# Kernel optimization log

Measured on AMD Instinct MI355X. Metric: run time of the kernel, lower is better.

The kernel has to match this reference:

```python
import jax, jax.numpy as jnp
import numpy as np

L = 8          # number of QTT cores = log2(init_reso)
RESO = 256     # init_reso
MAX_RANK = 256
N_SAMPLES = 4096


def _qtt_ranks(L, max_rank):
    return [min(8 ** k, 8 ** (L - k), max_rank) for k in range(L + 1)]


def setup_inputs() -> dict:
    key = jax.random.key(0)
    ranks = _qtt_ranks(L, MAX_RANK)
    keys = jax.random.split(key, L + 1)
    inp = {}
    for l in range(L):
        shape = (ranks[l], 8, ranks[l + 1])
        scale = (shape[0] * shape[1]) ** -0.5  # keep chain products O(1)
        inp[f"core{l}"] = jax.random.normal(keys[l], shape, dtype=jnp.float32) * scale
    inp["coords_xyz"] = jax.random.randint(keys[L], (N_SAMPLES, 3), 0, RESO)
    return inp


def _coords_to_qtt(coords_xyz, num_cores):
    # coords_xyz: (N, 3) int. Per core l (most-significant bit first):
    # c_l = 4*bit_x + 2*bit_y + bit_z in [0, 8)  -> shape (L, N)
    x, y, z = coords_xyz[:, 0], coords_xyz[:, 1], coords_xyz[:, 2]
    shifts = jnp.arange(num_cores - 1, -1, -1)[:, None]  # (L, 1)
    bx = (x[None, :] >> shifts) & 1
    by = (y[None, :] >> shifts) & 1
    bz = (z[None, :] >> shifts) & 1
    return 4 * bx + 2 * by + bz


def _sample_tt(cores, coords):
    # cores[l]: (r_l, 8, r_{l+1}); coords: (L, N)
    # v starts as first core slice: (N, r_1)  (r_0 == 1)
    v = cores[0][0, coords[0], :]
    for l in range(1, len(cores)):
        # gathered slice: (r_l, N, r_{l+1}) -> (N, r_l, r_{l+1})
        g = jnp.transpose(cores[l][:, coords[l], :], (1, 0, 2))
        v = jnp.einsum('nr,nrs->ns', v, g)
    return v[:, 0]  # r_L == 1 -> (N,)


def reference(core0, core1, core2, core3, core4, core5, core6, core7, coords_xyz):
    cores = [core0, core1, core2, core3, core4, core5, core6, core7]
    coords = _coords_to_qtt(coords_xyz, len(cores))
    return _sample_tt(cores, coords)
```

## Files before the change

kernel.cpp:

```cpp
#include <hip/hip_runtime.h>


typedef unsigned int u32;

__device__ __forceinline__ void fma4(float4& c, float a, const float4& b) {
    c.x = fmaf(a, b.x, c.x); c.y = fmaf(a, b.y, c.y);
    c.z = fmaf(a, b.z, c.z); c.w = fmaf(a, b.w, c.w);
}
__device__ __forceinline__ int digit_of(int x, int y, int z, int sh) {
    return 4*((x>>sh)&1) + 2*((y>>sh)&1) + ((z>>sh)&1);
}

__global__ __launch_bounds__(256, 4) void prep_kernel(
    const float* __restrict__ C4, float* __restrict__ C4t)
{
    const int t = threadIdx.x;
    const int cb = blockIdx.x;
    const int d4 = cb >> 3, s5o = cb & 7;
#pragma unroll 8
    for (int j = 0; j < 32; ++j) {
        const int s5 = s5o*32 + j;
        C4t[(size_t)d4*65536 + (size_t)s5*256 + t] =
            C4[(size_t)t*2048 + d4*256 + s5];
    }
}

__device__ __forceinline__ void comp8(
    const float (*As)[260], int kk,
    const float4& b0, const float4& b1, const float4& b2, const float4& b3,
    float4* acc)
{
#pragma unroll
    for (int r = 0; r < 8; ++r) {
        const float4 a = *(const float4*)&As[r][kk];
        fma4(acc[r], a.x, b0); fma4(acc[r], a.y, b1);
        fma4(acc[r], a.z, b2); fma4(acc[r], a.w, b3);
    }
}

template<int ROWSTRIDE>
__device__ __forceinline__ void kgemm8(
    const float* __restrict__ Bg,
    const float (*As)[260], int kbase, int ln, float4* acc)
{
    const float* gp = Bg + (size_t)kbase * ROWSTRIDE + (size_t)ln * 4;
    float4 bA0 = *(const float4*)(gp + (size_t)0*ROWSTRIDE);
    float4 bA1 = *(const float4*)(gp + (size_t)1*ROWSTRIDE);
    float4 bA2 = *(const float4*)(gp + (size_t)2*ROWSTRIDE);
    float4 bA3 = *(const float4*)(gp + (size_t)3*ROWSTRIDE);
    float4 bB0 = *(const float4*)(gp + (size_t)4*ROWSTRIDE);
    float4 bB1 = *(const float4*)(gp + (size_t)5*ROWSTRIDE);
    float4 bB2 = *(const float4*)(gp + (size_t)6*ROWSTRIDE);
    float4 bB3 = *(const float4*)(gp + (size_t)7*ROWSTRIDE);

#pragma unroll 1
    for (int s = 0; s < 8; ++s) {
        const int k0 = s * 8;
        comp8(As, kbase + k0, bA0, bA1, bA2, bA3, acc);
        if (s < 7) {
            bA0 = *(const float4*)(gp + (size_t)(k0+ 8)*ROWSTRIDE);
            bA1 = *(const float4*)(gp + (size_t)(k0+ 9)*ROWSTRIDE);
            bA2 = *(const float4*)(gp + (size_t)(k0+10)*ROWSTRIDE);
            bA3 = *(const float4*)(gp + (size_t)(k0+11)*ROWSTRIDE);
        }
        comp8(As, kbase + k0 + 4, bB0, bB1, bB2, bB3, acc);
        if (s < 7) {
            bB0 = *(const float4*)(gp + (size_t)(k0+12)*ROWSTRIDE);
            bB1 = *(const float4*)(gp + (size_t)(k0+13)*ROWSTRIDE);
            bB2 = *(const float4*)(gp + (size_t)(k0+14)*ROWSTRIDE);
            bB3 = *(const float4*)(gp + (size_t)(k0+15)*ROWSTRIDE);
        }
    }
}

__global__ __launch_bounds__(256, 2) void tables_kernel(
    const float* __restrict__ C0, const float* __restrict__ C1,
    const float* __restrict__ C2, const float* __restrict__ C3,
    const float* __restrict__ C4t, const float* __restrict__ C5,
    const float* __restrict__ C6, const float* __restrict__ C7,
    float* __restrict__ P3, float* __restrict__ U)
{
    __shared__ __align__(16) union {
        struct { float small[8][64]; float As[8][260]; } g;
        float red[4][4][256];
    } u;
    const int t = threadIdx.x;
    const int ln = t & 63, wv = t >> 6;
    const int bx = blockIdx.x;

    float4 acc[8];
#pragma unroll
    for (int r = 0; r < 8; ++r) acc[r] = make_float4(0,0,0,0);

    int rowBase, rowStep;
    float* outP;

    if (bx < 512) {
        const int d3 = bx & 7, d2 = (bx >> 3) & 7, d0 = bx >> 6;

#pragma unroll
        for (int j = 0; j < 2; ++j) {
            const int idx = t + 256*j, d1 = idx >> 6, c = idx & 63;
            float a = 0.f;
#pragma unroll
            for (int r8 = 0; r8 < 8; ++r8)
                a = fmaf(C0[d0*8 + r8], C1[r8*512 + d1*64 + c], a);
            u.g.small[d1][c] = a;
        }
        __syncthreads();

        {
            float4 a0 = make_float4(0,0,0,0), a1 = make_float4(0,0,0,0);
            const float* c2base = C2 + d2*256 + ln*4;
#pragma unroll 8
            for (int j = 0; j < 64; ++j) {
                const float4 c2 = *(const float4*)(c2base + (size_t)j*2048);
                fma4(a0, u.g.small[wv*2 + 0][j], c2);
                fma4(a1, u.g.small[wv*2 + 1][j], c2);
            }
            *(float4*)&u.g.As[wv*2 + 0][ln*4] = a0;
            *(float4*)&u.g.As[wv*2 + 1][ln*4] = a1;
        }
        __syncthreads();

        kgemm8<2048>(C3 + d3*256, u.g.As, wv*64, ln, acc);

        rowBase = d0*512 + d2*8 + d3; rowStep = 64;
        outP = P3;
    } else {
        const int ub = bx - 512;
        const int qt = ub & 63, d4 = ub >> 6;
        const int d5 = qt >> 3, d6 = qt & 7;

#pragma unroll
        for (int j = 0; j < 2; ++j) {
            const int idx = t + 256*j, r = idx >> 6, s6 = idx & 63;
            float a = 0.f;
#pragma unroll
            for (int jj = 0; jj < 8; ++jj)
                a = fmaf(C6[s6*64 + d6*8 + jj], C7[jj*8 + r], a);
            u.g.small[r][s6] = a;
        }
        __syncthreads();

        {
            float accT[8];
#pragma unroll
            for (int r = 0; r < 8; ++r) accT[r] = 0.f;
#pragma unroll
            for (int j4 = 0; j4 < 16; ++j4) {
                const float4 c5 = *(const float4*)(C5 + (size_t)t*512
                                                   + d5*64 + j4*4);
#pragma unroll
                for (int r = 0; r < 8; ++r) {
                    const float4 s6v = *(const float4*)&u.g.small[r][j4*4];
                    accT[r] = fmaf(c5.x, s6v.x, accT[r]);
                    accT[r] = fmaf(c5.y, s6v.y, accT[r]);
                    accT[r] = fmaf(c5.z, s6v.z, accT[r]);
                    accT[r] = fmaf(c5.w, s6v.w, accT[r]);
                }
            }
#pragma unroll
            for (int r = 0; r < 8; ++r) u.g.As[r][t] = accT[r];
        }
        __syncthreads();

        kgemm8<256>(C4t + (size_t)d4*65536, u.g.As, wv*64, ln, acc);

        rowBase = d4*512 + qt*8; rowStep = 1;
        outP = U;
    }

    __syncthreads();

#pragma unroll
    for (int ph = 0; ph < 2; ++ph) {
#pragma unroll
        for (int i = 0; i < 4; ++i)
            *(float4*)&u.red[wv][i][ln*4] = acc[ph*4 + i];
        __syncthreads();
        {
            float4 v        = *(const float4*)&u.red[0][wv][ln*4];
            const float4 p1 = *(const float4*)&u.red[1][wv][ln*4];
            const float4 p2 = *(const float4*)&u.red[2][wv][ln*4];
            const float4 p3 = *(const float4*)&u.red[3][wv][ln*4];
            v.x += p1.x + p2.x + p3.x; v.y += p1.y + p2.y + p3.y;
            v.z += p1.z + p2.z + p3.z; v.w += p1.w + p2.w + p3.w;
            const int r = ph*4 + wv;
            *(float4*)(outP + (size_t)(rowBase + rowStep*r)*256 + ln*4) = v;
        }
        __syncthreads();
    }
}

__global__ __launch_bounds__(256) void final_kernel(
    const float* __restrict__ P3, const float* __restrict__ U,
    const int* __restrict__ coords, int n, float* __restrict__ out)
{
    const int ln = threadIdx.x & 63, wv = threadIdx.x >> 6;
    const int s0 = blockIdx.x * 16 + wv * 4;

    float p[4] = {0.f, 0.f, 0.f, 0.f};
    int valid[4];
#pragma unroll
    for (int i = 0; i < 4; ++i) {
        const int s = s0 + i;
        valid[i] = (s < n);
        if (valid[i]) {
            const int x = coords[3*s], y = coords[3*s+1], z = coords[3*s+2];
            const int a  = digit_of(x,y,z,7)*512 + digit_of(x,y,z,6)*64
                         + digit_of(x,y,z,5)*8  + digit_of(x,y,z,4);
            const int d4 = digit_of(x,y,z,3);
            const int q  = digit_of(x,y,z,2)*64 + digit_of(x,y,z,1)*8
                         + digit_of(x,y,z,0);
            const float4 p4 = *(const float4*)(P3 + (size_t)a*256 + ln*4);
            const float4 u4 = *(const float4*)(U + (size_t)(d4*512 + q)*256 + ln*4);
            p[i] = fmaf(p4.x, u4.x, fmaf(p4.y, u4.y,
                   fmaf(p4.z, u4.z, p4.w * u4.w)));
        }
    }
#pragma unroll
    for (int m = 1; m <= 32; m <<= 1) {
        p[0] += __shfl_xor(p[0], m);
        p[1] += __shfl_xor(p[1], m);
        p[2] += __shfl_xor(p[2], m);
        p[3] += __shfl_xor(p[3], m);
    }
    if (ln == 0) {
#pragma unroll
        for (int i = 0; i < 4; ++i)
            if (valid[i]) out[s0 + i] = p[i];
    }
}

extern "C" void kernel_launch(void* const* d_in, const int* in_sizes, int n_in,
                              void* d_out, int out_size, void* d_ws, size_t ws_size,
                              hipStream_t stream) {
    const float* C0 = (const float*)d_in[0];
    const float* C1 = (const float*)d_in[1];
    const float* C2 = (const float*)d_in[2];
    const float* C3 = (const float*)d_in[3];
    const float* C4 = (const float*)d_in[4];
    const float* C5 = (const float*)d_in[5];
    const float* C6 = (const float*)d_in[6];
    const float* C7 = (const float*)d_in[7];
    const int* coords = (const int*)d_in[8];
    float* out = (float*)d_out;

    const int n = in_sizes[8] / 3;

    float* P3  = (float*)d_ws;
    float* U   = P3 + 4096*256;
    float* C4t = U  + 4096*256;

    prep_kernel<<<64, 256, 0, stream>>>(C4, C4t);
    tables_kernel<<<1024, 256, 0, stream>>>(
        C0, C1, C2, C3, C4t, C5, C6, C7, P3, U);
    final_kernel<<<(n + 15) / 16, 256, 0, stream>>>(P3, U, coords, n, out);
}
```

Baseline: 107.0 us.

## Split tables kernel output columns in half to double block count

```diff
diff --git a/kernel.cpp b/kernel.cpp
--- a/kernel.cpp
+++ b/kernel.cpp
@@ -6,6 +6,9 @@
 __device__ __forceinline__ void fma4(float4& c, float a, const float4& b) {
     c.x = fmaf(a, b.x, c.x); c.y = fmaf(a, b.y, c.y);
     c.z = fmaf(a, b.z, c.z); c.w = fmaf(a, b.w, c.w);
+}
+__device__ __forceinline__ void fma2(float2& c, float a, const float2& b) {
+    c.x = fmaf(a, b.x, c.x); c.y = fmaf(a, b.y, c.y);
 }
 __device__ __forceinline__ int digit_of(int x, int y, int z, int sh) {
     return 4*((x>>sh)&1) + 2*((y>>sh)&1) + ((z>>sh)&1);
@@ -25,50 +28,50 @@
     }
 }
 
-__device__ __forceinline__ void comp8(
+__device__ __forceinline__ void comp8h(
     const float (*As)[260], int kk,
-    const float4& b0, const float4& b1, const float4& b2, const float4& b3,
-    float4* acc)
+    const float2& b0, const float2& b1, const float2& b2, const float2& b3,
+    float2* acc)
 {
 #pragma unroll
     for (int r = 0; r < 8; ++r) {
         const float4 a = *(const float4*)&As[r][kk];
-        fma4(acc[r], a.x, b0); fma4(acc[r], a.y, b1);
-        fma4(acc[r], a.z, b2); fma4(acc[r], a.w, b3);
+        fma2(acc[r], a.x, b0); fma2(acc[r], a.y, b1);
+        fma2(acc[r], a.z, b2); fma2(acc[r], a.w, b3);
     }
 }
 
 template<int ROWSTRIDE>
-__device__ __forceinline__ void kgemm8(
-    const float* __restrict__ Bg,
-    const float (*As)[260], int kbase, int ln, float4* acc)
-{
-    const float* gp = Bg + (size_t)kbase * ROWSTRIDE + (size_t)ln * 4;
-    float4 bA0 = *(const float4*)(gp + (size_t)0*ROWSTRIDE);
-    float4 bA1 = *(const float4*)(gp + (size_t)1*ROWSTRIDE);
-    float4 bA2 = *(const float4*)(gp + (size_t)2*ROWSTRIDE);
-    float4 bA3 = *(const float4*)(gp + (size_t)3*ROWSTRIDE);
-    float4 bB0 = *(const float4*)(gp + (size_t)4*ROWSTRIDE);
-    float4 bB1 = *(const float4*)(gp + (size_t)5*ROWSTRIDE);
-    float4 bB2 = *(const float4*)(gp + (size_t)6*ROWSTRIDE);
-    float4 bB3 = *(const float4*)(gp + (size_t)7*ROWSTRIDE);
+__device__ __forceinline__ void kgemm8h(
+    const float* __restrict__ Bg, int colOff,
+    const float (*As)[260], int kbase, int ln, float2* acc)
+{
+    const float* gp = Bg + (size_t)kbase * ROWSTRIDE + colOff + (size_t)ln * 2;
+    float2 bA0 = *(const float2*)(gp + (size_t)0*ROWSTRIDE);
+    float2 bA1 = *(const float2*)(gp + (size_t)1*ROWSTRIDE);
+    float2 bA2 = *(const float2*)(gp + (size_t)2*ROWSTRIDE);
+    float2 bA3 = *(const float2*)(gp + (size_t)3*ROWSTRIDE);
+    float2 bB0 = *(const float2*)(gp + (size_t)4*ROWSTRIDE);
+    float2 bB1 = *(const float2*)(gp + (size_t)5*ROWSTRIDE);
+    float2 bB2 = *(const float2*)(gp + (size_t)6*ROWSTRIDE);
+    float2 bB3 = *(const float2*)(gp + (size_t)7*ROWSTRIDE);
 
 #pragma unroll 1
     for (int s = 0; s < 8; ++s) {
         const int k0 = s * 8;
-        comp8(As, kbase + k0, bA0, bA1, bA2, bA3, acc);
+        comp8h(As, kbase + k0, bA0, bA1, bA2, bA3, acc);
         if (s < 7) {
-            bA0 = *(const float4*)(gp + (size_t)(k0+ 8)*ROWSTRIDE);
-            bA1 = *(const float4*)(gp + (size_t)(k0+ 9)*ROWSTRIDE);
-            bA2 = *(const float4*)(gp + (size_t)(k0+10)*ROWSTRIDE);
-            bA3 = *(const float4*)(gp + (size_t)(k0+11)*ROWSTRIDE);
-        }
-        comp8(As, kbase + k0 + 4, bB0, bB1, bB2, bB3, acc);
+            bA0 = *(const float2*)(gp + (size_t)(k0+ 8)*ROWSTRIDE);
+            bA1 = *(const float2*)(gp + (size_t)(k0+ 9)*ROWSTRIDE);
+            bA2 = *(const float2*)(gp + (size_t)(k0+10)*ROWSTRIDE);
+            bA3 = *(const float2*)(gp + (size_t)(k0+11)*ROWSTRIDE);
+        }
+        comp8h(As, kbase + k0 + 4, bB0, bB1, bB2, bB3, acc);
         if (s < 7) {
-            bB0 = *(const float4*)(gp + (size_t)(k0+12)*ROWSTRIDE);
-            bB1 = *(const float4*)(gp + (size_t)(k0+13)*ROWSTRIDE);
-            bB2 = *(const float4*)(gp + (size_t)(k0+14)*ROWSTRIDE);
-            bB3 = *(const float4*)(gp + (size_t)(k0+15)*ROWSTRIDE);
+            bB0 = *(const float2*)(gp + (size_t)(k0+12)*ROWSTRIDE);
+            bB1 = *(const float2*)(gp + (size_t)(k0+13)*ROWSTRIDE);
+            bB2 = *(const float2*)(gp + (size_t)(k0+14)*ROWSTRIDE);
+            bB3 = *(const float2*)(gp + (size_t)(k0+15)*ROWSTRIDE);
         }
     }
 }
@@ -82,21 +85,23 @@
 {
     __shared__ __align__(16) union {
         struct { float small[8][64]; float As[8][260]; } g;
-        float red[4][4][256];
+        float red[4][4][128];
     } u;
     const int t = threadIdx.x;
     const int ln = t & 63, wv = t >> 6;
     const int bx = blockIdx.x;
 
-    float4 acc[8];
-#pragma unroll
-    for (int r = 0; r < 8; ++r) acc[r] = make_float4(0,0,0,0);
-
-    int rowBase, rowStep;
+    float2 acc[8];
+#pragma unroll
+    for (int r = 0; r < 8; ++r) acc[r] = make_float2(0.f, 0.f);
+
+    int rowBase, rowStep, colOff;
     float* outP;
 
-    if (bx < 512) {
-        const int d3 = bx & 7, d2 = (bx >> 3) & 7, d0 = bx >> 6;
+    if (bx < 1024) {
+        const int d3 = bx & 7, d2 = (bx >> 3) & 7;
+        const int hc = (bx >> 6) & 1, d0 = bx >> 7;
+        colOff = hc * 128;
 
 #pragma unroll
         for (int j = 0; j < 2; ++j) {
@@ -123,14 +128,15 @@
         }
         __syncthreads();
 
-        kgemm8<2048>(C3 + d3*256, u.g.As, wv*64, ln, acc);
+        kgemm8h<2048>(C3 + d3*256, colOff, u.g.As, wv*64, ln, acc);
 
         rowBase = d0*512 + d2*8 + d3; rowStep = 64;
         outP = P3;
     } else {
-        const int ub = bx - 512;
-        const int qt = ub & 63, d4 = ub >> 6;
+        const int ub = bx - 1024;
+        const int qt = ub & 63, hc = (ub >> 6) & 1, d4 = ub >> 7;
         const int d5 = qt >> 3, d6 = qt & 7;
+        colOff = hc * 128;
 
 #pragma unroll
         for (int j = 0; j < 2; ++j) {
@@ -165,7 +171,7 @@
         }
         __syncthreads();
 
-        kgemm8<256>(C4t + (size_t)d4*65536, u.g.As, wv*64, ln, acc);
+        kgemm8h<256>(C4t + (size_t)d4*65536, colOff, u.g.As, wv*64, ln, acc);
 
         rowBase = d4*512 + qt*8; rowStep = 1;
         outP = U;
@@ -177,17 +183,17 @@
     for (int ph = 0; ph < 2; ++ph) {
 #pragma unroll
         for (int i = 0; i < 4; ++i)
-            *(float4*)&u.red[wv][i][ln*4] = acc[ph*4 + i];
+            *(float2*)&u.red[wv][i][ln*2] = acc[ph*4 + i];
         __syncthreads();
         {
-            float4 v        = *(const float4*)&u.red[0][wv][ln*4];
-            const float4 p1 = *(const float4*)&u.red[1][wv][ln*4];
-            const float4 p2 = *(const float4*)&u.red[2][wv][ln*4];
-            const float4 p3 = *(const float4*)&u.red[3][wv][ln*4];
+            float2 v        = *(const float2*)&u.red[0][wv][ln*2];
+            const float2 p1 = *(const float2*)&u.red[1][wv][ln*2];
+            const float2 p2 = *(const float2*)&u.red[2][wv][ln*2];
+            const float2 p3 = *(const float2*)&u.red[3][wv][ln*2];
             v.x += p1.x + p2.x + p3.x; v.y += p1.y + p2.y + p3.y;
-            v.z += p1.z + p2.z + p3.z; v.w += p1.w + p2.w + p3.w;
             const int r = ph*4 + wv;
-            *(float4*)(outP + (size_t)(rowBase + rowStep*r)*256 + ln*4) = v;
+            *(float2*)(outP + (size_t)(rowBase + rowStep*r)*256
+                       + colOff + ln*2) = v;
         }
         __syncthreads();
     }
@@ -254,7 +260,7 @@
     float* C4t = U  + 4096*256;
 
     prep_kernel<<<64, 256, 0, stream>>>(C4, C4t);
-    tables_kernel<<<1024, 256, 0, stream>>>(
+    tables_kernel<<<2048, 256, 0, stream>>>(
         C0, C1, C2, C3, C4t, C5, C6, C7, P3, U);
     final_kernel<<<(n + 15) / 16, 256, 0, stream>>>(P3, U, coords, n, out);
 }
```

New measurement: 118.4 us. +10.6%, slower.
